# Performance work log

Measured on AMD Instinct MI355X. Metric: run time of the kernel, lower is better.

Reference implementation:

```python
import jax, jax.numpy as jnp
import numpy as np

B, H, D, HD = 16384, 8, 256, 128  # batch, heads, dim, hidden_dim


def setup_inputs() -> dict:
    key = jax.random.key(0)
    ks = jax.random.split(key, 8)
    return {
        "x": jax.random.normal(ks[0], (B, D), dtype=jnp.float32),
        "h": jax.random.normal(ks[1], (B, H, HD), dtype=jnp.float32),
        "sigmoid_w": jax.random.normal(ks[2], (H, HD + D, 2), dtype=jnp.float32),
        "sigmoid_b": jax.random.normal(ks[3], (H, 2), dtype=jnp.float32),
        "tanh_w": jax.random.normal(ks[4], (H, HD + D, HD), dtype=jnp.float32),
        "tanh_b": jax.random.normal(ks[5], (H, HD), dtype=jnp.float32),
        "out_w": jax.random.normal(ks[6], (H, HD, D), dtype=jnp.float32),
        "out_b": jax.random.normal(ks[7], (H, D), dtype=jnp.float32),
    }


def reference(x, h, sigmoid_w, sigmoid_b, tanh_w, tanh_b, out_w, out_b):
    # x: [B, D] -> broadcast across heads: [B, H, D]
    x_ = jnp.broadcast_to(x[:, None, :], (x.shape[0], h.shape[1], x.shape[1]))
    # gate input: [B, H, hidden+dim]
    sig_in = jnp.concatenate([h, x_], axis=2)
    sigmoids = jax.nn.sigmoid(jnp.einsum('bhm,hmn->bhn', sig_in, sigmoid_w) + sigmoid_b)
    # reset-gated hidden concat with x: [B, H, hidden+dim]
    tanh_in = jnp.concatenate([sigmoids[:, :, :1] * h, x_], axis=2)
    cand = jnp.tanh(jnp.einsum('bhm,hmn->bhn', tanh_in, tanh_w) + tanh_b)
    proportion = sigmoids[:, :, 1:]
    new_h = (1 - proportion) * h + proportion * cand
    output = jnp.einsum('bhm,hmn->bhn', new_h, out_w) + out_b
    return (output, new_h)
```

## Files before the change

kernel.cpp:

```cpp
#include <hip/hip_runtime.h>
#include <math.h>

typedef short bf16x8 __attribute__((ext_vector_type(8)));
typedef short bf16x4 __attribute__((ext_vector_type(4)));
typedef float floatx4 __attribute__((ext_vector_type(4)));
typedef float floatx2 __attribute__((ext_vector_type(2)));
typedef float floatx16 __attribute__((ext_vector_type(16)));

#define NB   16384
#define H8   8
#define ND   256
#define NHD  128
#define NK   384

__device__ __forceinline__ unsigned short f2bf(float f) {
  unsigned int u = __float_as_uint(f);
  u += 0x7FFFu + ((u >> 16) & 1u);
  return (unsigned short)(u >> 16);
}
__device__ __forceinline__ float bf2f(unsigned short s) {
  return __uint_as_float(((unsigned int)s) << 16);
}
__device__ __forceinline__ float fast_sigmoid(float z) {
  z = fminf(fmaxf(z, -60.f), 60.f);
  return __builtin_amdgcn_rcpf(1.f + __expf(-z));
}
__device__ __forceinline__ float fast_tanh(float s) {
  s = fminf(fmaxf(s, -9.f), 9.f);
  float e = __expf(2.f * s);
  return (e - 1.f) * __builtin_amdgcn_rcpf(e + 1.f);
}
__device__ __forceinline__ int swz(int idx16) {
  return idx16 ^ ((idx16 >> 6) & 7);
}

#define WTP (H8 * 24 * 4 * 512)
#define WOP (H8 * 8 * 8 * 512)
#define XFP (NB * ND)
#define NGATE (NB * H8)
#define WS_NEED3 ((size_t)(WTP + WOP + XFP) * 2 + (size_t)2 * NGATE * 4)

__global__ void prep3c(const float* __restrict__ tanh_w,
                       const float* __restrict__ sig_w,
                       const float* __restrict__ sig_b,
                       const float* __restrict__ out_w,
                       const float* __restrict__ x,
                       const float* __restrict__ h,
                       short* __restrict__ wtp_hi,
                       short* __restrict__ wop,
                       short* __restrict__ xfh,
                       float* __restrict__ gW, float* __restrict__ pW) {
  __shared__ float smem[14480];
  const int t = threadIdx.x;
  const int b = blockIdx.x;
  if (b < 192) {
    float* tile = smem;
    int head = b / 24, ks = b % 24;
    const float* slab = tanh_w + ((size_t)head * NK + ks * 16) * NHD;
#pragma unroll
    for (int it = 0; it < 2; ++it) {
      int i = it * 256 + t;
      floatx4 v = reinterpret_cast<const floatx4*>(slab)[i];
      int r = i >> 5, c4 = i & 31;
      *reinterpret_cast<floatx4*>(&tile[r * 132 + c4 * 4]) = v;
    }
    __syncthreads();
    int ct = t >> 6, l = t & 63;
    bf16x8 hi8;
#pragma unroll
    for (int j = 0; j < 8; ++j) {
      float w = tile[((l >> 5) * 8 + j) * 132 + ct * 32 + (l & 31)];
      hi8[j] = (short)f2bf(w);
    }
    size_t dst = ((((size_t)head * 24 + ks) * 4 + ct) * 64 + l) * 8;
    *reinterpret_cast<bf16x8*>(wtp_hi + dst) = hi8;
  } else if (b < 256) {
    float* tile = smem;
    int head = (b - 192) / 8, ks = (b - 192) % 8;
    const float* slab = out_w + ((size_t)head * NHD + ks * 16) * ND;
#pragma unroll
    for (int it = 0; it < 4; ++it) {
      int i = it * 256 + t;
      floatx4 v = reinterpret_cast<const floatx4*>(slab)[i];
      int r = i >> 6, c4 = i & 63;
      *reinterpret_cast<floatx4*>(&tile[r * 260 + c4 * 4]) = v;
    }
    __syncthreads();
#pragma unroll
    for (int u = 0; u < 2; ++u) {
      int idx = u * 256 + t;
      int ct = idx >> 6, l = idx & 63;
      bf16x8 o8;
#pragma unroll
      for (int j = 0; j < 8; ++j) {
        float w = tile[((l >> 5) * 8 + j) * 260 + ct * 32 + (l & 31)];
        o8[j] = (short)f2bf(w);
      }
      size_t dst = ((((size_t)head * 8 + ks) * 8 + ct) * 64 + l) * 8;
      *reinterpret_cast<bf16x8*>(wop + dst) = o8;
    }
  } else if (b < 2304) {
    int i = (b - 256) * 256 + t;
    int bb = i >> 5, c0 = (i & 31) * 8;
    const float* xp = x + (size_t)bb * ND + c0;
    floatx4 v0 = *reinterpret_cast<const floatx4*>(xp);
    floatx4 v1 = *reinterpret_cast<const floatx4*>(xp + 4);
    bf16x8 h8;
#pragma unroll
    for (int j = 0; j < 4; ++j) {
      h8[j] = (short)f2bf(v0[j]);
      h8[4 + j] = (short)f2bf(v1[j]);
    }
    int dst = ((bb >> 5) * 16 + (c0 >> 4)) * 512 +
              (((c0 >> 3) & 1) * 32 + (bb & 31)) * 8;
    *reinterpret_cast<bf16x8*>(xfh + dst) = h8;
  } else {
    float* xs = smem;
    float* ws = smem + 8320;
    int gb = b - 2304;
    long rowb = (long)gb * 32;
#pragma unroll
    for (int it = 0; it < 8; ++it) {
      int idx = it * 256 + t;
      int r = idx >> 6, c4 = idx & 63;
      floatx4 v = *reinterpret_cast<const floatx4*>(x + (rowb + r) * ND + c4 * 4);
      *reinterpret_cast<floatx4*>(&xs[r * 260 + c4 * 4]) = v;
    }
#pragma unroll
    for (int it = 0; it < 12; ++it) {
      int idx = it * 256 + t;
      floatx2 v = *reinterpret_cast<const floatx2*>(sig_w + (size_t)idx * 2);
      int head = idx / 384;
      int rem = idx * 2 - head * 768;
      *reinterpret_cast<floatx2*>(&ws[head * 770 + rem]) = v;
    }
    __syncthreads();
    int bl = t >> 3, head = t & 7;
    const float* hrow = h + (rowb * 8 + t) * 128;
    const float* wh = &ws[head * 770];
    float a0 = 0.f, a1 = 0.f;
#pragma unroll 8
    for (int k4 = 0; k4 < 32; ++k4) {
      floatx4 hv = *reinterpret_cast<const floatx4*>(hrow + k4 * 4);
#pragma unroll
      for (int j = 0; j < 4; ++j) {
        floatx2 w2 = *reinterpret_cast<const floatx2*>(&wh[(k4 * 4 + j) * 2]);
        a0 += hv[j] * w2[0];
        a1 += hv[j] * w2[1];
      }
    }
    const float* xrow = &xs[bl * 260];
#pragma unroll 8
    for (int k4 = 0; k4 < 64; ++k4) {
      floatx4 xv = *reinterpret_cast<const floatx4*>(xrow + k4 * 4);
#pragma unroll
      for (int j = 0; j < 4; ++j) {
        floatx2 w2 = *reinterpret_cast<const floatx2*>(&wh[(128 + k4 * 4 + j) * 2]);
        a0 += xv[j] * w2[0];
        a1 += xv[j] * w2[1];
      }
    }
    long gi = rowb * 8 + t;
    gW[gi] = fast_sigmoid(a0 + sig_b[head * 2 + 0]);
    pW[gi] = fast_sigmoid(a1 + sig_b[head * 2 + 1]);
  }
}

__global__ __launch_bounds__(256, 4) void gru3(
    const float* __restrict__ h,
    const float* __restrict__ tanh_b, const float* __restrict__ out_b,
    const short* __restrict__ wtp_hi, const short* __restrict__ wop,
    const short* __restrict__ xfh,
    const float* __restrict__ gW, const float* __restrict__ pW,
    float* __restrict__ out, float* __restrict__ out_nh) {
  __shared__ __align__(16) short AhH[16 * 512];
  __shared__ __align__(16) short AhL[16 * 512];
  __shared__ float pbuf[64], ginv[64];

  const int t = threadIdx.x;
  const int lane = t & 63;
  const int cq = t >> 6;
  const int l31 = lane & 31;
  const int lh = lane >> 5;
  const int head = (int)(blockIdx.x >> 8);
  const int rb = (int)(blockIdx.x & 255);
  const long rowbase = (long)rb * 64;

  if (t < 64) {
    pbuf[t] = pW[(rowbase + t) * H8 + head];
    float g = gW[(rowbase + t) * H8 + head];
    ginv[t] = __builtin_amdgcn_rcpf(fmaxf(g, 1e-30f));
  }

#pragma unroll
  for (int it = 0; it < 4; ++it) {
    int gi = it * 256 + t;
    int row = gi >> 4, kc = gi & 15;
    float g = gW[(rowbase + row) * H8 + head];
    const float* hp = h + ((rowbase + row) * H8 + head) * NHD + kc * 8;
    floatx4 v0 = *reinterpret_cast<const floatx4*>(hp);
    floatx4 v1 = *reinterpret_cast<const floatx4*>(hp + 4);
    bf16x8 hi8, lo8;
#pragma unroll
    for (int j = 0; j < 4; ++j) {
      float s0 = g * v0[j];
      unsigned short hb = f2bf(s0);
      hi8[j] = (short)hb; lo8[j] = (short)f2bf(s0 - bf2f(hb));
      float s1 = g * v1[j];
      unsigned short hb2 = f2bf(s1);
      hi8[4 + j] = (short)hb2; lo8[4 + j] = (short)f2bf(s1 - bf2f(hb2));
    }
    int rg = row >> 5, row32 = row & 31;
    int chunk = (rg * 8 + (kc >> 1)) * 64 + (kc & 1) * 32 + row32;
    int sc = swz(chunk);
    *reinterpret_cast<bf16x8*>(&AhH[sc * 8]) = hi8;
    *reinterpret_cast<bf16x8*>(&AhL[sc * 8]) = lo8;
  }
  __syncthreads();

  const short* __restrict__ xh0 = xfh + ((size_t)(rb * 2 + 0) * 16 * 512) + lane * 8;
  const short* __restrict__ xh1 = xfh + ((size_t)(rb * 2 + 1) * 16 * 512) + lane * 8;
  const short* __restrict__ bh_p = wtp_hi + (((size_t)head * 24 * 4 + cq) * 512) + lane * 8;

  floatx16 acc0, acc1;
#pragma unroll
  for (int z = 0; z < 16; ++z) { acc0[z] = 0.f; acc1[z] = 0.f; }

  bf16x8 bhA = *reinterpret_cast<const bf16x8*>(bh_p);
  bf16x8 bhB = *reinterpret_cast<const bf16x8*>(bh_p + 2048);
#pragma unroll
  for (int ks = 0; ks < 8; ++ks) {
    bf16x8 bh = bhA; bhA = bhB;
    bhB = *reinterpret_cast<const bf16x8*>(bh_p + (ks + 2) * 2048);
    bf16x8 a0h = *reinterpret_cast<const bf16x8*>(&AhH[swz(ks * 64 + lane) * 8]);
    bf16x8 a0l = *reinterpret_cast<const bf16x8*>(&AhL[swz(ks * 64 + lane) * 8]);
    bf16x8 a1h = *reinterpret_cast<const bf16x8*>(&AhH[swz((8 + ks) * 64 + lane) * 8]);
    bf16x8 a1l = *reinterpret_cast<const bf16x8*>(&AhL[swz((8 + ks) * 64 + lane) * 8]);
    acc0 = __builtin_amdgcn_mfma_f32_32x32x16_bf16(a0h, bh, acc0, 0, 0, 0);
    acc0 = __builtin_amdgcn_mfma_f32_32x32x16_bf16(a0l, bh, acc0, 0, 0, 0);
    acc1 = __builtin_amdgcn_mfma_f32_32x32x16_bf16(a1h, bh, acc1, 0, 0, 0);
    acc1 = __builtin_amdgcn_mfma_f32_32x32x16_bf16(a1l, bh, acc1, 0, 0, 0);
  }
  {
    bf16x8 x0A = *reinterpret_cast<const bf16x8*>(xh0);
    bf16x8 x1A = *reinterpret_cast<const bf16x8*>(xh1);
    bf16x8 x0B = *reinterpret_cast<const bf16x8*>(xh0 + 512);
    bf16x8 x1B = *reinterpret_cast<const bf16x8*>(xh1 + 512);
#pragma unroll
    for (int xk = 0; xk < 16; ++xk) {
      const int ks = 8 + xk;
      bf16x8 bh = bhA; bhA = bhB;
      if (ks + 2 < 24) bhB = *reinterpret_cast<const bf16x8*>(bh_p + (ks + 2) * 2048);
      bf16x8 x0 = x0A, x1 = x1A;
      x0A = x0B; x1A = x1B;
      if (xk + 2 < 16) {
        x0B = *reinterpret_cast<const bf16x8*>(xh0 + (xk + 2) * 512);
        x1B = *reinterpret_cast<const bf16x8*>(xh1 + (xk + 2) * 512);
      }
      acc0 = __builtin_amdgcn_mfma_f32_32x32x16_bf16(x0, bh, acc0, 0, 0, 0);
      acc1 = __builtin_amdgcn_mfma_f32_32x32x16_bf16(x1, bh, acc1, 0, 0, 0);
    }
  }
  __syncthreads();

  const int col = cq * 32 + l31;
  const float tb = tanh_b[head * NHD + col];
#define EPI(RG, ACC)                                                          \
  {                                                                           \
    _Pragma("unroll")                                                         \
    for (int reg = 0; reg < 16; ++reg) {                                      \
      int crow = (reg & 3) + 8 * (reg >> 2) + 4 * lh;                         \
      int row = RG * 32 + crow;                                               \
      float p = pbuf[row];                                                    \
      float cand = fast_tanh(ACC[reg] + tb);                                  \
      int el16 = (RG * 8 + (col >> 4)) * 64 + ((l31 >> 3) & 1) * 32 + crow;   \
      int eb = swz(el16) * 8 + (col & 7);                                     \
      float hv = (bf2f((unsigned short)AhH[eb]) +                             \
                  bf2f((unsigned short)AhL[eb])) * ginv[row];                 \
      float nh = hv + p * (cand - hv);                                        \
      out_nh[((rowbase + row) * H8 + head) * NHD + col] = nh;                 \
      AhH[eb] = (short)f2bf(nh);                                              \
    }                                                                         \
  }
  EPI(0, acc0)
  EPI(1, acc1)
#undef EPI
  __syncthreads();

  const short* __restrict__ wo_p = wop + (((size_t)head * 64 + cq * 2) * 512) + lane * 8;
  const float ob0 = out_b[head * ND + cq * 64 + l31];
  const float ob1 = out_b[head * ND + cq * 64 + 32 + l31];
#define OUTP(RG)                                                              \
  {                                                                           \
    floatx16 a3a, a3b;                                                        \
    _Pragma("unroll")                                                         \
    for (int z = 0; z < 16; ++z) { a3a[z] = 0.f; a3b[z] = 0.f; }              \
    bf16x8 w0n = *reinterpret_cast<const bf16x8*>(wo_p);                      \
    bf16x8 w1n = *reinterpret_cast<const bf16x8*>(wo_p + 512);                \
    _Pragma("unroll")                                                         \
    for (int ks = 0; ks < 8; ++ks) {                                          \
      bf16x8 w0 = w0n, w1 = w1n;                                              \
      if (ks < 7) {                                                           \
        w0n = *reinterpret_cast<const bf16x8*>(wo_p + (ks + 1) * 4096);       \
        w1n = *reinterpret_cast<const bf16x8*>(wo_p + (ks + 1) * 4096 + 512); \
      }                                                                       \
      bf16x8 a = *reinterpret_cast<const bf16x8*>(&AhH[swz((RG * 8 + ks) * 64 + lane) * 8]); \
      a3a = __builtin_amdgcn_mfma_f32_32x32x16_bf16(a, w0, a3a, 0, 0, 0);     \
      a3b = __builtin_amdgcn_mfma_f32_32x32x16_bf16(a, w1, a3b, 0, 0, 0);     \
    }                                                                         \
    _Pragma("unroll")                                                         \
    for (int reg = 0; reg < 16; ++reg) {                                      \
      int row = RG * 32 + (reg & 3) + 8 * (reg >> 2) + 4 * lh;                \
      long obase = ((rowbase + row) * H8 + head) * ND;                        \
      out[obase + cq * 64 + l31] = a3a[reg] + ob0;                            \
      out[obase + cq * 64 + 32 + l31] = a3b[reg] + ob1;                       \
    }                                                                         \
  }
  OUTP(0)
  OUTP(1)
#undef OUTP
}

#define WT_ELEMS (H8 * NK * NHD)
#define WO_ELEMS (H8 * NHD * ND)

__global__ void prep_kernel(const float* __restrict__ tanh_w,
                            const float* __restrict__ out_w,
                            short* __restrict__ wt_hi,
                            short* __restrict__ wt_lo,
                            short* __restrict__ wo) {
  const int total1 = WT_ELEMS;
  const int total2 = WO_ELEMS;
  for (int i = blockIdx.x * blockDim.x + threadIdx.x; i < total1 + total2;
       i += gridDim.x * blockDim.x) {
    if (i < total1) {
      int hh = i / (NK * NHD);
      int rem = i - hh * NK * NHD;
      int k = rem / NHD, n = rem - k * NHD;
      float w = tanh_w[i];
      unsigned short hi = f2bf(w);
      unsigned short lo = f2bf(w - bf2f(hi));
      int dst = hh * (48 * NHD * 8) + (k >> 3) * (NHD * 8) + n * 8 + (k & 7);
      wt_hi[dst] = (short)hi;
      wt_lo[dst] = (short)lo;
    } else {
      int j = i - total1;
      int hh = j / (NHD * ND);
      int rem = j - hh * NHD * ND;
      int k = rem / ND, n = rem - k * ND;
      int dst = hh * (16 * ND * 8) + (k >> 3) * (ND * 8) + n * 8 + (k & 7);
      wo[dst] = (short)f2bf(out_w[j]);
    }
  }
}

#define BM   32
#define NT   512
#define LDA 392
#define LDNH 136

__global__ __launch_bounds__(NT, 4) void gru_main(
    const float* __restrict__ x, const float* __restrict__ h,
    const float* __restrict__ sig_w, const float* __restrict__ sig_b,
    const float* __restrict__ tanh_b, const float* __restrict__ out_b,
    const short* __restrict__ wt_hi, const short* __restrict__ wt_lo,
    const short* __restrict__ wo,
    float* __restrict__ out, float* __restrict__ out_nh) {
  __shared__ __align__(16) short Ahi[BM][LDA];
  __shared__ __align__(16) short Alo[BM][LDA];
  __shared__ __align__(16) short NHL[BM][LDNH];
  __shared__ floatx2 swl[NK];
  __shared__ float gbuf[BM], pbuf[BM];

  const int t = threadIdx.x;
  const int lane = t & 63;
  const int wid = t >> 6;
  const int wrow = wid >> 2;
  const int wcol = wid & 3;
  const int ln = lane & 15;
  const int kg = lane >> 4;
  const int head = blockIdx.x & 7;
  const long rowbase = (long)(blockIdx.x >> 3) * BM;
  const int arow = wrow * 16 + ln;

#pragma unroll
  for (int i = 0; i < 4; ++i) {
    int idx = i * NT + t;
    int r = idx >> 6, c4 = idx & 63;
    floatx4 v = *reinterpret_cast<const floatx4*>(x + (rowbase + r) * ND + c4 * 4);
    bf16x4 hi, lo;
#pragma unroll
    for (int j = 0; j < 4; ++j) {
      unsigned short hb = f2bf(v[j]);
      hi[j] = (short)hb;
      lo[j] = (short)f2bf(v[j] - bf2f(hb));
    }
    *reinterpret_cast<bf16x4*>(&Ahi[r][NHD + c4 * 4]) = hi;
    *reinterpret_cast<bf16x4*>(&Alo[r][NHD + c4 * 4]) = lo;
  }
#pragma unroll
  for (int i = 0; i < 2; ++i) {
    int idx = i * NT + t;
    int r = idx >> 5, c4 = idx & 31;
    floatx4 v = *reinterpret_cast<const floatx4*>(
        h + ((rowbase + r) * H8 + head) * NHD + c4 * 4);
    bf16x4 hi, lo;
#pragma unroll
    for (int j = 0; j < 4; ++j) {
      unsigned short hb = f2bf(v[j]);
      hi[j] = (short)hb;
      lo[j] = (short)f2bf(v[j] - bf2f(hb));
    }
    *reinterpret_cast<bf16x4*>(&Ahi[r][c4 * 4]) = hi;
    *reinterpret_cast<bf16x4*>(&Alo[r][c4 * 4]) = lo;
  }
  if (t < NK)
    swl[t] = *reinterpret_cast<const floatx2*>(sig_w + ((size_t)head * NK + t) * 2);
  __syncthreads();
  {
    int r = t >> 4, u = t & 15;
    float a0 = 0.f, a1 = 0.f;
#pragma unroll
    for (int kk = 0; kk < 24; ++kk) {
      int k = u + kk * 16;
      float a = bf2f((unsigned short)Ahi[r][k]) + bf2f((unsigned short)Alo[r][k]);
      floatx2 w = swl[k];
      a0 += a * w[0];
      a1 += a * w[1];
    }
#pragma unroll
    for (int off = 1; off < 16; off <<= 1) {
      a0 += __shfl_xor(a0, off);
      a1 += __shfl_xor(a1, off);
    }
    if (u == 0) {
      gbuf[r] = fast_sigmoid(a0 + sig_b[head * 2 + 0]);
      pbuf[r] = fast_sigmoid(a1 + sig_b[head * 2 + 1]);
    }
  }
  floatx4 acc1[2] = {{0.f, 0.f, 0.f, 0.f}, {0.f, 0.f, 0.f, 0.f}};
  floatx4 acc2[2] = {{0.f, 0.f, 0.f, 0.f}, {0.f, 0.f, 0.f, 0.f}};
  const size_t wtbase = (size_t)head * (48 * NHD * 8);
#pragma unroll
  for (int ks = 0; ks < 12; ++ks) {
    bf16x8 ahi = *reinterpret_cast<const bf16x8*>(&Ahi[arow][ks * 32 + kg * 8]);
    bf16x8 alo = *reinterpret_cast<const bf16x8*>(&Alo[arow][ks * 32 + kg * 8]);
    floatx4* acc = (ks < 4) ? acc1 : acc2;
#pragma unroll
    for (int cf = 0; cf < 2; ++cf) {
      int n0 = wcol * 32 + cf * 16;
      size_t woff = wtbase + (size_t)(ks * 4 + kg) * (NHD * 8) + (size_t)(n0 + ln) * 8;
      bf16x8 bhi = *reinterpret_cast<const bf16x8*>(wt_hi + woff);
      bf16x8 blo = *reinterpret_cast<const bf16x8*>(wt_lo + woff);
      acc[cf] = __builtin_amdgcn_mfma_f32_16x16x32_bf16(ahi, bhi, acc[cf], 0, 0, 0);
      acc[cf] = __builtin_amdgcn_mfma_f32_16x16x32_bf16(alo, bhi, acc[cf], 0, 0, 0);
      acc[cf] = __builtin_amdgcn_mfma_f32_16x16x32_bf16(ahi, blo, acc[cf], 0, 0, 0);
    }
  }
  __syncthreads();
#pragma unroll
  for (int cf = 0; cf < 2; ++cf) {
    int col = wcol * 32 + cf * 16 + ln;
    float tb = tanh_b[head * NHD + col];
#pragma unroll
    for (int j = 0; j < 4; ++j) {
      int r = wrow * 16 + kg * 4 + j;
      float g = gbuf[r], p = pbuf[r];
      float s = g * acc1[cf][j] + acc2[cf][j] + tb;
      float cand = fast_tanh(s);
      float hv = bf2f((unsigned short)Ahi[r][col]) + bf2f((unsigned short)Alo[r][col]);
      float nh = hv + p * (cand - hv);
      out_nh[((rowbase + r) * H8 + head) * NHD + col] = nh;
      NHL[r][col] = (short)f2bf(nh);
    }
  }
  __syncthreads();
  floatx4 acc3[4] = {{0.f, 0.f, 0.f, 0.f}, {0.f, 0.f, 0.f, 0.f},
                     {0.f, 0.f, 0.f, 0.f}, {0.f, 0.f, 0.f, 0.f}};
  const size_t wobase = (size_t)head * (16 * ND * 8);
#pragma unroll
  for (int ks = 0; ks < 4; ++ks) {
    bf16x8 a = *reinterpret_cast<const bf16x8*>(&NHL[arow][ks * 32 + kg * 8]);
#pragma unroll
    for (int cf = 0; cf < 4; ++cf) {
      int n0 = wcol * 64 + cf * 16;
      size_t woff = wobase + (size_t)(ks * 4 + kg) * (ND * 8) + (size_t)(n0 + ln) * 8;
      bf16x8 bfr = *reinterpret_cast<const bf16x8*>(wo + woff);
      acc3[cf] = __builtin_amdgcn_mfma_f32_16x16x32_bf16(a, bfr, acc3[cf], 0, 0, 0);
    }
  }
#pragma unroll
  for (int cf = 0; cf < 4; ++cf) {
    int col = wcol * 64 + cf * 16 + ln;
    float ob = out_b[head * ND + col];
#pragma unroll
    for (int j = 0; j < 4; ++j) {
      int r = wrow * 16 + kg * 4 + j;
      out[((rowbase + r) * H8 + head) * ND + col] = acc3[cf][j] + ob;
    }
  }
}

extern "C" void kernel_launch(void* const* d_in, const int* in_sizes, int n_in,
                              void* d_out, int out_size, void* d_ws, size_t ws_size,
                              hipStream_t stream) {
  (void)in_sizes; (void)n_in; (void)out_size;
  const float* x      = (const float*)d_in[0];
  const float* h      = (const float*)d_in[1];
  const float* sig_w  = (const float*)d_in[2];
  const float* sig_b  = (const float*)d_in[3];
  const float* tanh_w = (const float*)d_in[4];
  const float* tanh_b = (const float*)d_in[5];
  const float* out_w  = (const float*)d_in[6];
  const float* out_b  = (const float*)d_in[7];

  float* out = (float*)d_out;
  float* out_nh = out + (size_t)NB * H8 * ND;

  if (ws_size >= WS_NEED3) {
    short* wtp_hi = (short*)d_ws;
    short* wop    = wtp_hi + WTP;
    short* xfh    = wop + WOP;
    float* gW     = (float*)(xfh + XFP);
    float* pW     = gW + NGATE;
    hipLaunchKernelGGL(prep3c, dim3(256 + 2048 + 512), dim3(256), 0, stream,
                       tanh_w, sig_w, sig_b, out_w, x, h,
                       wtp_hi, wop, xfh, gW, pW);
    hipLaunchKernelGGL(gru3, dim3((NB / 64) * H8), dim3(256), 0, stream,
                       h, tanh_b, out_b, wtp_hi, wop, xfh, gW, pW,
                       out, out_nh);
  } else {
    short* wt_hi = (short*)d_ws;
    short* wt_lo = wt_hi + WT_ELEMS;
    short* wo    = wt_lo + WT_ELEMS;
    hipLaunchKernelGGL(prep_kernel, dim3(512), dim3(256), 0, stream,
                       tanh_w, out_w, wt_hi, wt_lo, wo);
    hipLaunchKernelGGL(gru_main, dim3((NB / BM) * H8), dim3(NT), 0, stream,
                       x, h, sig_w, sig_b, tanh_b, out_b, wt_hi, wt_lo, wo,
                       out, out_nh);
  }
}
```

Baseline: 85.66 us.

## Fuse x bf16 conversion into gate blocks and drop gate smem staging

Removes the separate 2048-block x-to-bf16 conversion phase in the prep kernel. The gate-computation blocks, which already stage x rows in shared memory, now also emit the bf16 xfh layout from that copy, so x is read from global memory once instead of twice. In the main kernel the pbuf/ginv shared arrays are removed and gate values are loaded directly from global (cached) memory in the epilogue, with the reciprocal recomputed per element. Launch bounds are raised from 4 to 5 blocks per SM to allow more occupancy, at the risk of register spills and extra global loads in the epilogue.

New measurement: 99.34 us. 1.16x slower.

```diff
diff --git a/kernel.cpp b/kernel.cpp
--- a/kernel.cpp
+++ b/kernel.cpp
@@ -99,25 +99,10 @@
       size_t dst = ((((size_t)head * 8 + ks) * 8 + ct) * 64 + l) * 8;
       *reinterpret_cast<bf16x8*>(wop + dst) = o8;
     }
-  } else if (b < 2304) {
-    int i = (b - 256) * 256 + t;
-    int bb = i >> 5, c0 = (i & 31) * 8;
-    const float* xp = x + (size_t)bb * ND + c0;
-    floatx4 v0 = *reinterpret_cast<const floatx4*>(xp);
-    floatx4 v1 = *reinterpret_cast<const floatx4*>(xp + 4);
-    bf16x8 h8;
-#pragma unroll
-    for (int j = 0; j < 4; ++j) {
-      h8[j] = (short)f2bf(v0[j]);
-      h8[4 + j] = (short)f2bf(v1[j]);
-    }
-    int dst = ((bb >> 5) * 16 + (c0 >> 4)) * 512 +
-              (((c0 >> 3) & 1) * 32 + (bb & 31)) * 8;
-    *reinterpret_cast<bf16x8*>(xfh + dst) = h8;
   } else {
     float* xs = smem;
     float* ws = smem + 8320;
-    int gb = b - 2304;
+    int gb = b - 256;
     long rowb = (long)gb * 32;
 #pragma unroll
     for (int it = 0; it < 8; ++it) {
@@ -135,6 +120,20 @@
       *reinterpret_cast<floatx2*>(&ws[head * 770 + rem]) = v;
     }
     __syncthreads();
+
+#pragma unroll
+    for (int it = 0; it < 4; ++it) {
+      int idx = it * 256 + t;
+      int bl2 = idx >> 5, c0 = (idx & 31) * 8;
+      bf16x8 h8;
+#pragma unroll
+      for (int j = 0; j < 8; ++j)
+        h8[j] = (short)f2bf(xs[bl2 * 260 + c0 + j]);
+      int dst = (gb * 16 + (c0 >> 4)) * 512 +
+                (((c0 >> 3) & 1) * 32 + bl2) * 8;
+      *reinterpret_cast<bf16x8*>(xfh + dst) = h8;
+    }
+
     int bl = t >> 3, head = t & 7;
     const float* hrow = h + (rowb * 8 + t) * 128;
     const float* wh = &ws[head * 770];
@@ -166,7 +165,7 @@
   }
 }
 
-__global__ __launch_bounds__(256, 4) void gru3(
+__global__ __launch_bounds__(256, 5) void gru3(
     const float* __restrict__ h,
     const float* __restrict__ tanh_b, const float* __restrict__ out_b,
     const short* __restrict__ wtp_hi, const short* __restrict__ wop,
@@ -175,7 +174,6 @@
     float* __restrict__ out, float* __restrict__ out_nh) {
   __shared__ __align__(16) short AhH[16 * 512];
   __shared__ __align__(16) short AhL[16 * 512];
-  __shared__ float pbuf[64], ginv[64];
 
   const int t = threadIdx.x;
   const int lane = t & 63;
@@ -185,18 +183,14 @@
   const int head = (int)(blockIdx.x >> 8);
   const int rb = (int)(blockIdx.x & 255);
   const long rowbase = (long)rb * 64;
-
-  if (t < 64) {
-    pbuf[t] = pW[(rowbase + t) * H8 + head];
-    float g = gW[(rowbase + t) * H8 + head];
-    ginv[t] = __builtin_amdgcn_rcpf(fmaxf(g, 1e-30f));
-  }
+  const float* __restrict__ gRow = gW + rowbase * H8 + head;
+  const float* __restrict__ pRow = pW + rowbase * H8 + head;
 
 #pragma unroll
   for (int it = 0; it < 4; ++it) {
     int gi = it * 256 + t;
     int row = gi >> 4, kc = gi & 15;
-    float g = gW[(rowbase + row) * H8 + head];
+    float g = gRow[(size_t)row * H8];
     const float* hp = h + ((rowbase + row) * H8 + head) * NHD + kc * 8;
     floatx4 v0 = *reinterpret_cast<const floatx4*>(hp);
     floatx4 v1 = *reinterpret_cast<const floatx4*>(hp + 4);
@@ -271,12 +265,13 @@
     for (int reg = 0; reg < 16; ++reg) {                                      \
       int crow = (reg & 3) + 8 * (reg >> 2) + 4 * lh;                         \
       int row = RG * 32 + crow;                                               \
-      float p = pbuf[row];                                                    \
+      float p = pRow[(size_t)row * H8];                                       \
+      float gi_ = __builtin_amdgcn_rcpf(fmaxf(gRow[(size_t)row * H8], 1e-30f)); \
       float cand = fast_tanh(ACC[reg] + tb);                                  \
       int el16 = (RG * 8 + (col >> 4)) * 64 + ((l31 >> 3) & 1) * 32 + crow;   \
       int eb = swz(el16) * 8 + (col & 7);                                     \
       float hv = (bf2f((unsigned short)AhH[eb]) +                             \
-                  bf2f((unsigned short)AhL[eb])) * ginv[row];                 \
+                  bf2f((unsigned short)AhL[eb])) * gi_;                       \
       float nh = hv + p * (cand - hv);                                        \
       out_nh[((rowbase + row) * H8 + head) * NHD + col] = nh;                 \
       AhH[eb] = (short)f2bf(nh);                                              \
@@ -523,7 +518,7 @@
     short* xfh    = wop + WOP;
     float* gW     = (float*)(xfh + XFP);
     float* pW     = gW + NGATE;
-    hipLaunchKernelGGL(prep3c, dim3(256 + 2048 + 512), dim3(256), 0, stream,
+    hipLaunchKernelGGL(prep3c, dim3(256 + 512), dim3(256), 0, stream,
                        tanh_w, sig_w, sig_b, out_w, x, h,
                        wtp_hi, wop, xfh, gW, pW);
     hipLaunchKernelGGL(gru3, dim3((NB / 64) * H8), dim3(256), 0, stream,
```
